# Kernel optimization log

Hardware: AMD Instinct MI355X
Metric: run time of the kernel (lower is better)

The kernel has to match this reference:

```python
import jax, jax.numpy as jnp
import numpy as np

N_HEADS = 16
ROPE_BASE = 10000.0


def _rope_tables(T, head_dim, dtype):
    inv_freq = 1.0 / (ROPE_BASE ** (jnp.arange(0, head_dim, 2, dtype=jnp.float32) / head_dim))
    t = jnp.arange(T, dtype=jnp.float32)
    freqs = jnp.outer(t, inv_freq)              # (T, head_dim/2)
    emb = jnp.concatenate([freqs, freqs], -1)   # (T, head_dim)
    return jnp.cos(emb).astype(dtype), jnp.sin(emb).astype(dtype)


def _rotate_half(x):
    x1, x2 = jnp.split(x, 2, axis=-1)
    return jnp.concatenate([-x2, x1], axis=-1)


def setup_inputs() -> dict:
    key = jax.random.key(0)
    k1, k2, k3 = jax.random.split(key, 3)
    B, T, C = 2, 2048, 2048
    x = jax.random.normal(k1, (B, T, C), dtype=jnp.float32)
    Wqkv = jax.random.normal(k2, (C, 3 * C), dtype=jnp.float32) * (1.0 / np.sqrt(C))
    Wproj = jax.random.normal(k3, (C, C), dtype=jnp.float32) * (1.0 / np.sqrt(C))
    return {"x": x, "Wqkv": Wqkv, "Wproj": Wproj}


def reference(x, Wqkv, Wproj):
    B, T, C = x.shape
    H = N_HEADS
    D = C // H
    qkv = jnp.einsum('btc,cd->btd', x, Wqkv)            # (B,T,3C)
    q, k, v = jnp.split(qkv, 3, axis=-1)
    # (B,T,C) -> (B,H,T,D)
    q = q.reshape(B, T, H, D).transpose(0, 2, 1, 3)
    k = k.reshape(B, T, H, D).transpose(0, 2, 1, 3)
    v = v.reshape(B, T, H, D).transpose(0, 2, 1, 3)
    cos, sin = _rope_tables(T, D, x.dtype)              # (T,D) each
    q = q * cos + _rotate_half(q) * sin
    k = k * cos + _rotate_half(k) * sin
    scale = 1.0 / jnp.sqrt(jnp.asarray(D, x.dtype))
    att = jnp.einsum('bhqd,bhkd->bhqk', q, k) * scale   # (B,H,T,T)
    causal = jnp.tril(jnp.ones((T, T), dtype=bool))
    att = jnp.where(causal, att, jnp.asarray(-jnp.inf, att.dtype))
    att = jax.nn.softmax(att, axis=-1)
    y = jnp.einsum('bhqk,bhkd->bhqd', att, v)           # (B,H,T,D)
    y = y.transpose(0, 2, 1, 3).reshape(B, T, C)
    return jnp.einsum('btc,cd->btd', y, Wproj)
```

## Files before the change

kernel.cpp:

```cpp
#include <hip/hip_runtime.h>
#include <stdint.h>

#define T_SEQ 2048
#define NH 16
#define HD 128
#define CC 2048
#define N3 6144
#define MM 4096

typedef short bf16x8 __attribute__((ext_vector_type(8)));
typedef float f32x4 __attribute__((ext_vector_type(4)));
typedef float f32x16 __attribute__((ext_vector_type(16)));
typedef unsigned int u32x4 __attribute__((ext_vector_type(4)));

__device__ __forceinline__ unsigned short f2bf(float f) {
  unsigned int u = __float_as_uint(f);
  u += 0x7FFF + ((u >> 16) & 1);
  return (unsigned short)(u >> 16);
}
__device__ __forceinline__ float bf2f(unsigned short h) {
  return __uint_as_float(((unsigned int)h) << 16);
}
__device__ __forceinline__ unsigned int cvt_pk_bf16(float lo, float hi) {
  unsigned int r;
  asm("v_cvt_pk_bf16_f32 %0, %1, %2" : "=v"(r) : "v"(lo), "v"(hi));
  return r;
}

__global__ __launch_bounds__(256) void k_transpose_cvt(const float* __restrict__ in,
                                                       unsigned short* __restrict__ out,
                                                       int K, int N) {
  __shared__ float tile[32][33];
  int k0 = blockIdx.x * 32;
  int n0 = blockIdx.y * 32;
  int tx = threadIdx.x & 31, ty = threadIdx.x >> 5;
  #pragma unroll
  for (int r = ty; r < 32; r += 8)
    tile[r][tx] = in[(size_t)(k0 + r) * N + n0 + tx];
  __syncthreads();
  #pragma unroll
  for (int r = ty; r < 32; r += 8)
    out[(size_t)(n0 + r) * K + k0 + tx] = f2bf(tile[tx][r]);
}

__global__ __launch_bounds__(256) void k_cvt(const float* __restrict__ in,
                                             unsigned short* __restrict__ out, int n4) {
  int i = blockIdx.x * 256 + threadIdx.x;
  if (i >= n4) return;
  float4 v = ((const float4*)in)[i];
  ushort4 o;
  o.x = f2bf(v.x); o.y = f2bf(v.y); o.z = f2bf(v.z); o.w = f2bf(v.w);
  ((ushort4*)out)[i] = o;
}

template<int NJ, int EPI, int MMAJ>
__global__ __launch_bounds__(512, 1) void k_gemm8(const unsigned short* __restrict__ A,
                                                  const unsigned short* __restrict__ Bt,
                                                  float* __restrict__ C,
                                                  unsigned short* __restrict__ qo,
                                                  unsigned short* __restrict__ ko,
                                                  unsigned short* __restrict__ vto,
                                                  int M, int N, int K) {
  constexpr int BU = NJ / 2;
  constexpr int DSTRIDE = (1 + BU) * 16384;
  extern __shared__ __align__(16) char lds[];
  const int tid = threadIdx.x;
  const int lane = tid & 63;
  const int lr = lane & 15, lg = lane >> 4;
  const int wave = tid >> 6;
  const int wm = wave >> 2, wn = wave & 3;
  const int nwg = gridDim.x;
  const int bid = blockIdx.x;
  const int wg = (bid & 7) * (nwg >> 3) + (bid >> 3);
  const int GX = M >> 7;
  const int GN = N / (NJ * 64);
  const int mt = MMAJ ? (wg % GX) : (wg / GN);
  const int nt = MMAJ ? (wg / GX) : (wg % GN);
  const int m0 = mt * 128, n0 = nt * NJ * 64;
  const int NT = K >> 6;

  auto STAGE = [&](int d, int op, int h, int t) {
    const unsigned short* src = op ? Bt : A;
    const int r0 = (op ? n0 + h * 128 : m0);
    const int kc = t * 64;
    char* base = lds + d * DSTRIDE + op * 16384 + h * 16384;
    #pragma unroll
    for (int l = 0; l < 2; ++l) {
      int p = (l * 512 + tid) * 16;
      int qq = p ^ (((p >> 7) & 7) << 4);
      const unsigned short* g = src + (size_t)(r0 + (qq >> 7)) * K + kc + ((qq & 127) >> 1);
      __builtin_amdgcn_global_load_lds(
          (const __attribute__((address_space(1))) void*)g,
          (__attribute__((address_space(3))) void*)(base + (l * 512 + (tid & 448)) * 16),
          16, 0, 0);
    }
  };
  auto RD = [&](int d, int op, int row, int kb) -> bf16x8 {
    const char* base = lds + d * DSTRIDE + op * 16384;
    int p = row * 128 + kb;
    p ^= ((p >> 7) & 7) << 4;
    return *(const bf16x8*)(base + p);
  };

  f32x4 acc[4][NJ];
  #pragma unroll
  for (int i = 0; i < 4; ++i)
    #pragma unroll
    for (int j = 0; j < NJ; ++j) acc[i][j] = (f32x4){0.f, 0.f, 0.f, 0.f};

  bf16x8 bfrg[NJ][2];

#define GPH(D, MI, READB, DOST, SD, SO, SH, ST, VM)                                      \
  {                                                                                      \
    if (READB) {                                                                         \
      _Pragma("unroll")                                                                  \
      for (int nj = 0; nj < NJ; ++nj)                                                    \
        _Pragma("unroll")                                                                \
        for (int ks = 0; ks < 2; ++ks)                                                   \
          bfrg[nj][ks] = RD(D, 1, wn * NJ * 16 + nj * 16 + lr, ks * 64 + lg * 16);       \
    }                                                                                    \
    bf16x8 af[2];                                                                        \
    _Pragma("unroll")                                                                    \
    for (int ks = 0; ks < 2; ++ks)                                                       \
      af[ks] = RD(D, 0, wm * 64 + (MI) * 16 + lr, ks * 64 + lg * 16);                    \
    if (DOST) STAGE(SD, SO, SH, ST);                                                     \
    __builtin_amdgcn_s_barrier();                                                        \
    asm volatile("s_waitcnt lgkmcnt(0)" ::: "memory");                                   \
    __builtin_amdgcn_s_setprio(1);                                                       \
    _Pragma("unroll")                                                                    \
    for (int nj = 0; nj < NJ; ++nj)                                                      \
      _Pragma("unroll")                                                                  \
      for (int ks = 0; ks < 2; ++ks)                                                     \
        acc[MI][nj] = __builtin_amdgcn_mfma_f32_16x16x32_bf16(af[ks], bfrg[nj][ks], acc[MI][nj], 0, 0, 0); \
    __builtin_amdgcn_s_setprio(0);                                                       \
    if ((VM) == 6) asm volatile("s_waitcnt vmcnt(6)" ::: "memory");                      \
    if ((VM) == 4) asm volatile("s_waitcnt vmcnt(4)" ::: "memory");                      \
    __builtin_amdgcn_s_barrier();                                                        \
  }

#define GPM(D, MIB, READB, VM, ...)                                                      \
  {                                                                                      \
    if (READB) {                                                                         \
      _Pragma("unroll")                                                                  \
      for (int nj = 0; nj < NJ; ++nj)                                                    \
        _Pragma("unroll")                                                                \
        for (int ks = 0; ks < 2; ++ks)                                                   \
          bfrg[nj][ks] = RD(D, 1, wn * NJ * 16 + nj * 16 + lr, ks * 64 + lg * 16);       \
    }                                                                                    \
    bf16x8 af2[2][2];                                                                    \
    _Pragma("unroll")                                                                    \
    for (int mm = 0; mm < 2; ++mm)                                                       \
      _Pragma("unroll")                                                                  \
      for (int ks = 0; ks < 2; ++ks)                                                     \
        af2[mm][ks] = RD(D, 0, wm * 64 + (MIB + mm) * 16 + lr, ks * 64 + lg * 16);       \
    __VA_ARGS__                                                                          \
    __builtin_amdgcn_s_barrier();                                                        \
    asm volatile("s_waitcnt lgkmcnt(0)" ::: "memory");                                   \
    __builtin_amdgcn_s_setprio(1);                                                       \
    _Pragma("unroll")                                                                    \
    for (int mm = 0; mm < 2; ++mm)                                                       \
      _Pragma("unroll")                                                                  \
      for (int nj = 0; nj < NJ; ++nj)                                                    \
        _Pragma("unroll")                                                                \
        for (int ks = 0; ks < 2; ++ks)                                                   \
          acc[MIB + mm][nj] = __builtin_amdgcn_mfma_f32_16x16x32_bf16(af2[mm][ks], bfrg[nj][ks], acc[MIB + mm][nj], 0, 0, 0); \
    __builtin_amdgcn_s_setprio(0);                                                       \
    if ((VM) == 4) asm volatile("s_waitcnt vmcnt(4)" ::: "memory");                      \
    if ((VM) == 2) asm volatile("s_waitcnt vmcnt(2)" ::: "memory");                      \
    __builtin_amdgcn_s_barrier();                                                        \
  }

  const int t1 = NT > 1 ? 1 : 0;
  #pragma unroll
  for (int h = 0; h < BU; ++h) STAGE(0, 1, h, 0);
  STAGE(0, 0, 0, 0);
  #pragma unroll
  for (int h = 0; h < BU; ++h) STAGE(1, 1, h, t1);
  if (NJ == 6) asm volatile("s_waitcnt vmcnt(6)" ::: "memory");
  else         asm volatile("s_waitcnt vmcnt(4)" ::: "memory");
  __builtin_amdgcn_s_barrier();

  for (int it = 0; it < (NT >> 1); ++it) {
    const int tb  = 2 * it + 1;
    const int ta1 = min(2 * it + 2, NT - 1);
    const int tb1 = min(2 * it + 3, NT - 1);
    if constexpr (NJ == 6) {
      GPH(0, 0, true,  true, 1, 0, 0, tb,  -1)
      GPH(0, 1, false, true, 0, 1, 0, ta1, -1)
      GPH(0, 2, false, true, 0, 1, 1, ta1, -1)
      GPH(0, 3, false, true, 0, 1, 2, ta1,  6)
      GPH(1, 0, true,  true, 0, 0, 0, ta1, -1)
      GPH(1, 1, false, true, 1, 1, 0, tb1, -1)
      GPH(1, 2, false, true, 1, 1, 1, tb1, -1)
      GPH(1, 3, false, true, 1, 1, 2, tb1,  6)
    } else {
      GPM(0, 0, true,  -1, STAGE(1, 0, 0, tb);)
      GPM(0, 2, false,  2, STAGE(0, 1, 0, ta1);)
      GPM(1, 0, true,  -1, STAGE(0, 1, 1, ta1); STAGE(0, 0, 0, ta1);)
      GPM(1, 2, false,  4, STAGE(1, 1, 0, tb1); STAGE(1, 1, 1, tb1);)
    }
  }
#undef GPH
#undef GPM

  if (EPI == 0) {
    #pragma unroll
    for (int mi = 0; mi < 4; ++mi)
      #pragma unroll
      for (int nj = 0; nj < NJ; ++nj)
        #pragma unroll
        for (int j = 0; j < 4; ++j) {
          int m = m0 + wm * 64 + mi * 16 + lg * 4 + j;
          int n = n0 + wn * NJ * 16 + nj * 16 + lr;
          C[(size_t)m * N + n] = acc[mi][nj][j];
        }
  } else {
    const bool hasV = (n0 + NJ * 64 > 4096);
    if (hasV) __builtin_amdgcn_s_barrier();
    unsigned short* ldv = (unsigned short*)lds;
    #pragma unroll
    for (int mi = 0; mi < 4; ++mi) {
      #pragma unroll
      for (int nj = 0; nj < NJ; ++nj) {
        int lcol = wn * NJ * 16 + nj * 16 + lr;
        int n = n0 + lcol;
        int which = n >> 11, cc = n & 2047;
        int h = cc >> 7, d = cc & 127;
        int lrow = wm * 64 + mi * 16 + lg * 4;
        int m_base = m0 + lrow;
        int b = m_base >> 11, t = m_base & 2047;
        if (which == 2) {
          #pragma unroll
          for (int j = 0; j < 4; ++j)
            ldv[lcol * 136 + lrow + j] = f2bf(acc[mi][nj][j]);
        } else {
          unsigned short* dst = which == 0 ? qo : ko;
          #pragma unroll
          for (int j = 0; j < 4; ++j)
            dst[(((size_t)(b * NH + h)) * T_SEQ + t + j) * HD + d] = f2bf(acc[mi][nj][j]);
        }
      }
    }
    if (hasV) {
      __builtin_amdgcn_s_barrier();
      const int bb = m0 >> 11, t0 = m0 & 2047;
      for (int pass = 0; pass < (NJ * 64) / 32; ++pass) {
        int col = pass * 32 + (tid >> 4);
        int rg = tid & 15;
        int n = n0 + col;
        if ((n >> 11) == 2) {
          int cc = n & 2047, h = cc >> 7, d = cc & 127;
          bf16x8 vv = *(const bf16x8*)(ldv + col * 136 + rg * 8);
          *(bf16x8*)(vto + (((size_t)(bb * NH + h) * HD + d) * T_SEQ + t0 + rg * 8)) = vv;
        }
      }
    }
  }
}

__global__ __launch_bounds__(256) void k_rope(unsigned short* __restrict__ q,
                                              unsigned short* __restrict__ k) {
  int i = blockIdx.x * 256 + threadIdx.x;
  int d = i & 63;
  int t = (i >> 6) & (T_SEQ - 1);
  int bh = i >> 17;
  float invf = exp2f((float)(-2 * d) * (13.287712379549449f / 128.f));
  float ang = (float)t * invf;
  float c = cosf(ang), s = sinf(ang);
  size_t base = ((size_t)bh * T_SEQ + t) * HD + d;
  const float scale = 0.12751741562076117f;
  float q1 = bf2f(q[base]), q2 = bf2f(q[base + 64]);
  q[base]      = f2bf((q1 * c - q2 * s) * scale);
  q[base + 64] = f2bf((q2 * c + q1 * s) * scale);
  float k1 = bf2f(k[base]), k2 = bf2f(k[base + 64]);
  k[base]      = f2bf(k1 * c - k2 * s);
  k[base + 64] = f2bf(k2 * c + k1 * s);
}

__global__ __launch_bounds__(512, 1) void k_attn(const unsigned short* __restrict__ Q,
                                                 const unsigned short* __restrict__ K,
                                                 const unsigned short* __restrict__ Vt,
                                                 unsigned short* __restrict__ Y) {
  extern __shared__ __align__(16) char alds[];
  char* Kls = alds;
  char* Vls = alds + 65536;
  const int id = blockIdx.x;
  const int bh = id & 31;
  const int qtl = 15 - (id >> 5);
  const int b = bh >> 4, h = bh & 15;
  const int tid = threadIdx.x, wv = tid >> 6, lane = tid & 63;
  const int l31 = lane & 31, hh = lane >> 5;
  const int par = wv >> 2;
  const int wq = wv & 3;
  const int q0 = qtl * 128;
  const int qglob = q0 + wq * 32 + l31;
  const unsigned short* Qb = Q + (size_t)bh * T_SEQ * HD;
  const unsigned short* Kb = K + (size_t)bh * T_SEQ * HD;
  const unsigned short* Vb = Vt + (size_t)bh * HD * T_SEQ;

  auto STAGEK = [&](int tk, int s) {
    char* base = Kls + s * 16384;
    #pragma unroll
    for (int ch = 0; ch < 2; ++ch) {
      int p = (ch * 512 + tid) * 16;
      int q = p ^ (((p >> 8) & 7) << 4);
      const unsigned short* g = Kb + (size_t)(tk + (q >> 8)) * HD + ((q & 255) >> 1);
      __builtin_amdgcn_global_load_lds(
          (const __attribute__((address_space(1))) void*)g,
          (__attribute__((address_space(3))) void*)(base + (ch * 512 + (tid & 448)) * 16),
          16, 0, 0);
    }
  };
  auto STAGEV = [&](int tk, int s) {
    char* base = Vls + s * 16384;
    #pragma unroll
    for (int ch = 0; ch < 2; ++ch) {
      int p = (ch * 512 + tid) * 16;
      int q = p ^ (((p >> 7) & 7) << 4);
      const unsigned short* g = Vb + (size_t)(q >> 7) * T_SEQ + tk + ((q & 127) >> 1);
      __builtin_amdgcn_global_load_lds(
          (const __attribute__((address_space(1))) void*)g,
          (__attribute__((address_space(3))) void*)(base + (ch * 512 + (tid & 448)) * 16),
          16, 0, 0);
    }
  };

  bf16x8 qfr[8];
  #pragma unroll
  for (int c = 0; c < 8; ++c)
    qfr[c] = *(const bf16x8*)(Qb + (size_t)qglob * HD + c * 16 + hh * 8);

  f32x16 oacc[4];
  #pragma unroll
  for (int dt = 0; dt < 4; ++dt)
    #pragma unroll
    for (int r = 0; r < 16; ++r) oacc[dt][r] = 0.f;
  float mrun = -1e30f, lrun = 0.f;

  STAGEK(0, 0); STAGEV(0, 0);
  STAGEK(64, 1); STAGEV(64, 1);
  asm volatile("s_waitcnt vmcnt(0)" ::: "memory");
  __syncthreads();

  for (int u = 0; u <= qtl; ++u) {
    if (u < qtl) {
      STAGEK((2 * u + 2) * 64, (2 * u + 2) & 3); STAGEV((2 * u + 2) * 64, (2 * u + 2) & 3);
      STAGEK((2 * u + 3) * 64, (2 * u + 3) & 3); STAGEV((2 * u + 3) * 64, (2 * u + 3) & 3);
    }
    const int jt = 2 * u + par;
    const int slot = jt & 3;

    f32x16 sacc[2];
    #pragma unroll
    for (int t = 0; t < 2; ++t)
      #pragma unroll
      for (int r = 0; r < 16; ++r) sacc[t][r] = 0.f;
    {
      const char* kbase = Kls + slot * 16384;
      #pragma unroll
      for (int t = 0; t < 2; ++t) {
        bf16x8 kf8[8];
        #pragma unroll
        for (int s = 0; s < 8; ++s) {
          int row = t * 32 + l31;
          int byte = (row * 256 + s * 32 + hh * 16) ^ ((row & 7) << 4);
          kf8[s] = *(const bf16x8*)(kbase + byte);
        }
        __builtin_amdgcn_s_setprio(1);
        #pragma unroll
        for (int s = 0; s < 8; ++s)
          sacc[t] = __builtin_amdgcn_mfma_f32_32x32x16_bf16(kf8[s], qfr[s], sacc[t], 0, 0, 0);
        __builtin_amdgcn_s_setprio(0);
      }
    }

    if (jt >= 2 * qtl) {
      #pragma unroll
      for (int t = 0; t < 2; ++t)
        #pragma unroll
        for (int r = 0; r < 16; ++r) {
          int kg = jt * 64 + t * 32 + (r & 3) + 8 * (r >> 2) + 4 * hh;
          if (kg > qglob) sacc[t][r] = -1e30f;
        }
    }

    float pmax = sacc[0][0];
    #pragma unroll
    for (int r = 1; r < 16; ++r) pmax = fmaxf(pmax, sacc[0][r]);
    #pragma unroll
    for (int r = 0; r < 16; ++r) pmax = fmaxf(pmax, sacc[1][r]);
    pmax = fmaxf(pmax, __shfl_xor(pmax, 32));

    if (__any(pmax > mrun + 8.0f)) {
      float mnew = fmaxf(mrun, pmax);
      float osc = exp2f(mrun - mnew);
      lrun *= osc;
      mrun = mnew;
      #pragma unroll
      for (int r = 0; r < 16; ++r) {
        int qr = (r & 3) + 8 * (r >> 2) + 4 * hh;
        float sr = __shfl(osc, qr);
        #pragma unroll
        for (int dt = 0; dt < 4; ++dt) oacc[dt][r] *= sr;
      }
    }

    unsigned int pk[16];
    float rsum = 0.f;
    #pragma unroll
    for (int t = 0; t < 2; ++t)
      #pragma unroll
      for (int i = 0; i < 8; ++i) {
        float p0 = exp2f(sacc[t][2 * i] - mrun);
        float p1 = exp2f(sacc[t][2 * i + 1] - mrun);
        rsum += p0 + p1;
        pk[t * 8 + i] = cvt_pk_bf16(p0, p1);
      }
    rsum += __shfl_xor(rsum, 32);
    lrun += rsum;

    bf16x8 pa[4];
    #pragma unroll
    for (int c = 0; c < 4; ++c) {
      int base = (c >> 1) * 8 + (c & 1) * 4;
      unsigned int s0 = hh == 0 ? pk[base + 2] : pk[base + 0];
      unsigned int s1 = hh == 0 ? pk[base + 3] : pk[base + 1];
      unsigned int r0 = __shfl_xor((int)s0, 32);
      unsigned int r1 = __shfl_xor((int)s1, 32);
      u32x4 f;
      f[0] = hh == 0 ? pk[base + 0] : r0;
      f[1] = hh == 0 ? pk[base + 1] : r1;
      f[2] = hh == 0 ? r0 : pk[base + 2];
      f[3] = hh == 0 ? r1 : pk[base + 3];
      pa[c] = *(bf16x8*)&f;
    }

    {
      const char* vbase = Vls + slot * 16384;
      __builtin_amdgcn_s_setprio(1);
      #pragma unroll
      for (int dt = 0; dt < 4; ++dt) {
        #pragma unroll
        for (int c = 0; c < 4; ++c) {
          int row = dt * 32 + l31;
          int byte = (row * 128 + c * 32 + hh * 16) ^ ((row & 7) << 4);
          bf16x8 vf = *(const bf16x8*)(vbase + byte);
          oacc[dt] = __builtin_amdgcn_mfma_f32_32x32x16_bf16(pa[c], vf, oacc[dt], 0, 0, 0);
        }
      }
      __builtin_amdgcn_s_setprio(0);
    }

    asm volatile("s_waitcnt vmcnt(0)" ::: "memory");
    __syncthreads();
  }

  float* obuf  = (float*)alds;
  float* mlbuf = (float*)(alds + 65536);
  if (par == 1) {
    mlbuf[(wq * 64 + lane) * 2 + 0] = mrun;
    mlbuf[(wq * 64 + lane) * 2 + 1] = lrun;
    float* ob = obuf + wq * 4096;
    #pragma unroll
    for (int dt = 0; dt < 4; ++dt)
      #pragma unroll
      for (int r = 0; r < 16; ++r)
        ob[(dt * 16 + r) * 64 + lane] = oacc[dt][r];
  }
  __syncthreads();
  if (par == 0) {
    float mo = mlbuf[(wq * 64 + lane) * 2 + 0];
    float lo = mlbuf[(wq * 64 + lane) * 2 + 1];
    float mm = fmaxf(mrun, mo);
    float se = exp2f(mrun - mm), so = exp2f(mo - mm);
    float lt = lrun * se + lo * so;
    float linv = 1.0f / lt;
    const float* ob = obuf + wq * 4096;
    #pragma unroll
    for (int r = 0; r < 16; ++r) {
      int qr = (r & 3) + 8 * (r >> 2) + 4 * hh;
      float se_r = __shfl(se, qr);
      float so_r = __shfl(so, qr);
      float li_r = __shfl(linv, qr);
      int qg = q0 + wq * 32 + qr;
      size_t base = ((size_t)b * T_SEQ + qg) * CC + h * HD;
      #pragma unroll
      for (int dt = 0; dt < 4; ++dt) {
        float oo = ob[(dt * 16 + r) * 64 + lane];
        Y[base + dt * 32 + l31] = f2bf((oacc[dt][r] * se_r + oo * so_r) * li_r);
      }
    }
  }
}

extern "C" void kernel_launch(void* const* d_in, const int* in_sizes, int n_in,
                              void* d_out, int out_size, void* d_ws, size_t ws_size,
                              hipStream_t stream) {
  const float* x     = (const float*)d_in[0];
  const float* Wqkv  = (const float*)d_in[1];
  const float* Wproj = (const float*)d_in[2];
  float* out = (float*)d_out;
  char* ws = (char*)d_ws;
  const size_t MB = 1024 * 1024;
  unsigned short* WqkvT  = (unsigned short*)(ws + 0);
  unsigned short* WprojT = (unsigned short*)(ws + 24 * MB);
  unsigned short* xb     = (unsigned short*)(ws + 32 * MB);
  unsigned short* y      = xb;
  unsigned short* q      = (unsigned short*)(ws + 48 * MB);
  unsigned short* k      = (unsigned short*)(ws + 64 * MB);
  unsigned short* vt     = (unsigned short*)(ws + 80 * MB);

  k_transpose_cvt<<<dim3(CC / 32, N3 / 32), 256, 0, stream>>>(Wqkv, WqkvT, CC, N3);
  k_transpose_cvt<<<dim3(CC / 32, CC / 32), 256, 0, stream>>>(Wproj, WprojT, CC, CC);
  k_cvt<<<(MM * CC / 4) / 256, 256, 0, stream>>>(x, xb, MM * CC / 4);
  k_gemm8<6, 1, 1><<<dim3((MM / 128) * (N3 / 384)), 512, 131072, stream>>>(
      xb, WqkvT, nullptr, q, k, vt, MM, N3, CC);
  k_rope<<<(32 * T_SEQ * 64) / 256, 256, 0, stream>>>(q, k);
  k_attn<<<dim3(512), 512, 131072, stream>>>(q, k, vt, y);
  k_gemm8<4, 0, 0><<<dim3((MM / 128) * (CC / 256)), 512, 98304, stream>>>(
      y, WprojT, out, nullptr, nullptr, nullptr, MM, CC, CC);
}
```

Baseline: 252.3 us.

## Merge prep kernels into one launch and fuse Q RoPE into attention

Folds the two weight transpose-converts and the x conversion into a single k_prep launch to cut launch overhead and tail effects. Moves RoPE and softmax scaling for Q out of the standalone rope kernel and into k_attn, applied to the register-resident Q fragments right after loading, so the rope pass touches only K. The cost is per-thread sin/cos computation inside attention (64 elements per thread), which adds some latency before the main loop.

```diff
diff --git a/kernel.cpp b/kernel.cpp
--- a/kernel.cpp
+++ b/kernel.cpp
@@ -27,30 +27,41 @@
   return r;
 }
 
-__global__ __launch_bounds__(256) void k_transpose_cvt(const float* __restrict__ in,
-                                                       unsigned short* __restrict__ out,
-                                                       int K, int N) {
+__global__ __launch_bounds__(256) void k_prep(const float* __restrict__ Wqkv,
+                                              unsigned short* __restrict__ WqkvT,
+                                              const float* __restrict__ Wproj,
+                                              unsigned short* __restrict__ WprojT,
+                                              const float* __restrict__ x,
+                                              unsigned short* __restrict__ xb) {
   __shared__ float tile[32][33];
-  int k0 = blockIdx.x * 32;
-  int n0 = blockIdx.y * 32;
-  int tx = threadIdx.x & 31, ty = threadIdx.x >> 5;
-  #pragma unroll
-  for (int r = ty; r < 32; r += 8)
-    tile[r][tx] = in[(size_t)(k0 + r) * N + n0 + tx];
-  __syncthreads();
-  #pragma unroll
-  for (int r = ty; r < 32; r += 8)
-    out[(size_t)(n0 + r) * K + k0 + tx] = f2bf(tile[tx][r]);
-}
-
-__global__ __launch_bounds__(256) void k_cvt(const float* __restrict__ in,
-                                             unsigned short* __restrict__ out, int n4) {
-  int i = blockIdx.x * 256 + threadIdx.x;
-  if (i >= n4) return;
-  float4 v = ((const float4*)in)[i];
-  ushort4 o;
-  o.x = f2bf(v.x); o.y = f2bf(v.y); o.z = f2bf(v.z); o.w = f2bf(v.w);
-  ((ushort4*)out)[i] = o;
+  const int bi = blockIdx.x;
+  const int tx = threadIdx.x & 31, ty = threadIdx.x >> 5;
+  if (bi < 16384) {
+    const float* in;
+    unsigned short* out;
+    int k0, n0, N;
+    if (bi < 12288) {
+      in = Wqkv; out = WqkvT; N = N3;
+      k0 = (bi & 63) * 32; n0 = (bi >> 6) * 32;
+    } else {
+      in = Wproj; out = WprojT; N = CC;
+      int b2 = bi - 12288;
+      k0 = (b2 & 63) * 32; n0 = (b2 >> 6) * 32;
+    }
+    #pragma unroll
+    for (int r = ty; r < 32; r += 8)
+      tile[r][tx] = in[(size_t)(k0 + r) * N + n0 + tx];
+    __syncthreads();
+    #pragma unroll
+    for (int r = ty; r < 32; r += 8)
+      out[(size_t)(n0 + r) * CC + k0 + tx] = f2bf(tile[tx][r]);
+  } else {
+    int i = (bi - 16384) * 256 + threadIdx.x;
+    float4 v = ((const float4*)x)[i];
+    ushort4 o;
+    o.x = f2bf(v.x); o.y = f2bf(v.y); o.z = f2bf(v.z); o.w = f2bf(v.w);
+    ((ushort4*)xb)[i] = o;
+  }
 }
 
 template<int NJ, int EPI, int MMAJ>
@@ -258,8 +269,7 @@
   }
 }
 
-__global__ __launch_bounds__(256) void k_rope(unsigned short* __restrict__ q,
-                                              unsigned short* __restrict__ k) {
+__global__ __launch_bounds__(256) void k_ropek(unsigned short* __restrict__ k) {
   int i = blockIdx.x * 256 + threadIdx.x;
   int d = i & 63;
   int t = (i >> 6) & (T_SEQ - 1);
@@ -268,10 +278,6 @@
   float ang = (float)t * invf;
   float c = cosf(ang), s = sinf(ang);
   size_t base = ((size_t)bh * T_SEQ + t) * HD + d;
-  const float scale = 0.12751741562076117f;
-  float q1 = bf2f(q[base]), q2 = bf2f(q[base + 64]);
-  q[base]      = f2bf((q1 * c - q2 * s) * scale);
-  q[base + 64] = f2bf((q2 * c + q1 * s) * scale);
   float k1 = bf2f(k[base]), k2 = bf2f(k[base + 64]);
   k[base]      = f2bf(k1 * c - k2 * s);
   k[base + 64] = f2bf(k2 * c + k1 * s);
@@ -329,6 +335,23 @@
   #pragma unroll
   for (int c = 0; c < 8; ++c)
     qfr[c] = *(const bf16x8*)(Qb + (size_t)qglob * HD + c * 16 + hh * 8);
+  {
+    const float SCALE = 0.12751741562076117f;
+    const float L2I = 13.287712379549449f / 64.f;
+    #pragma unroll
+    for (int c = 0; c < 4; ++c) {
+      #pragma unroll
+      for (int e = 0; e < 8; ++e) {
+        int d = c * 16 + hh * 8 + e;
+        float ang = (float)qglob * exp2f(-(float)d * L2I);
+        float cs = cosf(ang), sn = sinf(ang);
+        float lo = bf2f((unsigned short)qfr[c][e]);
+        float hi = bf2f((unsigned short)qfr[c + 4][e]);
+        qfr[c][e]     = (short)f2bf((lo * cs - hi * sn) * SCALE);
+        qfr[c + 4][e] = (short)f2bf((hi * cs + lo * sn) * SCALE);
+      }
+    }
+  }
 
   f32x16 oacc[4];
   #pragma unroll
@@ -510,12 +533,10 @@
   unsigned short* k      = (unsigned short*)(ws + 64 * MB);
   unsigned short* vt     = (unsigned short*)(ws + 80 * MB);
 
-  k_transpose_cvt<<<dim3(CC / 32, N3 / 32), 256, 0, stream>>>(Wqkv, WqkvT, CC, N3);
-  k_transpose_cvt<<<dim3(CC / 32, CC / 32), 256, 0, stream>>>(Wproj, WprojT, CC, CC);
-  k_cvt<<<(MM * CC / 4) / 256, 256, 0, stream>>>(x, xb, MM * CC / 4);
+  k_prep<<<dim3(24576), 256, 0, stream>>>(Wqkv, WqkvT, Wproj, WprojT, x, xb);
   k_gemm8<6, 1, 1><<<dim3((MM / 128) * (N3 / 384)), 512, 131072, stream>>>(
       xb, WqkvT, nullptr, q, k, vt, MM, N3, CC);
-  k_rope<<<(32 * T_SEQ * 64) / 256, 256, 0, stream>>>(q, k);
+  k_ropek<<<(32 * T_SEQ * 64) / 256, 256, 0, stream>>>(k);
   k_attn<<<dim3(512), 512, 131072, stream>>>(q, k, vt, y);
   k_gemm8<4, 0, 0><<<dim3((MM / 128) * (CC / 256)), 512, 98304, stream>>>(
       y, WprojT, out, nullptr, nullptr, nullptr, MM, CC, CC);
```

Result: slower. 528.4 us (+109.4%).
